# Performance work log

Measured on AMD Instinct MI355X. Metric: run time of the kernel, lower is better.

Reference implementation:

```python
import jax, jax.numpy as jnp
import numpy as np

B_GRAPHS, N_PER, T = 64, 5, 256
F_NODE, F_GLOB = 64, 16
H_MSG, H_UPD, H_GRP, H_ACT = 128, 128, 64, 4


def _lstm(x, Wih, Whh, bih, bhh):
    """PyTorch-semantics single-layer LSTM, batch_first=False.
    x: [L, B, Din] -> out [L, B, H]. Scan runs over dim 0 (faithful to the
    original code, which feeds [edges/nodes, T, F] into nn.LSTM)."""
    H = Whh.shape[1]
    xz = jnp.einsum('lbd,gd->lbg', x, Wih) + (bih + bhh)  # precomputed input proj [L,B,4H]
    h0 = jnp.zeros((x.shape[1], H), x.dtype)

    def step(carry, zt):
        h, c = carry
        z = zt + h @ Whh.T
        i, f, g, o = jnp.split(z, 4, axis=-1)  # torch gate order: i,f,g,o
        c = jax.nn.sigmoid(f) * c + jax.nn.sigmoid(i) * jnp.tanh(g)
        h = jax.nn.sigmoid(o) * jnp.tanh(c)
        return (h, c), h

    _, ys = jax.lax.scan(step, (h0, h0), xz)
    return ys


def _forward(nodes, global_attr,
             Wih_m, Whh_m, bih_m, bhh_m,
             Wih_u, Whh_u, bih_u, bhh_u,
             Wih_g, Whh_g, bih_g, bhh_g,
             Wih_a, Whh_a, bih_a, bhh_a,
             edge_indices, num_nodes, num_edges, batch_indices, chosen_who):
    N, Tdim = nodes.shape[0], nodes.shape[1]
    E = edge_indices.shape[1]
    B = num_nodes.shape[0]
    # Faithful to source: both src and target use edge_indices[0]
    src = edge_indices[0]
    tgt = edge_indices[0]
    ga = global_attr.reshape(-1, Tdim, global_attr.shape[1])  # [B, T, G]

    # --- message phase: gather -> LSTM -> relu -> scatter_min ---
    glob_e = jnp.repeat(ga, num_edges, axis=0, total_repeat_length=E)  # [E,T,G]
    msg_in = jnp.concatenate([nodes[src], nodes[tgt], glob_e], axis=2)  # [E,T,2F+G]
    message = jax.nn.relu(_lstm(msg_in, Wih_m, Whh_m, bih_m, bhh_m))    # [E,T,Hm]
    aggr = jax.ops.segment_min(message, tgt, num_segments=N)            # [N,T,Hm]

    # --- node update ---
    glob_n = jnp.repeat(ga, num_nodes, axis=0, total_repeat_length=N)   # [N,T,G]
    upd_in = jnp.concatenate([nodes, aggr, glob_n], axis=2)
    upd = jax.nn.relu(_lstm(upd_in, Wih_u, Whh_u, bih_u, bhh_u))        # [N,T,Hu]

    # --- global / group embedding ---
    agg_nodes = jax.ops.segment_min(upd, batch_indices, num_segments=B) # [B,T,Hu]
    group = jax.nn.relu(_lstm(jnp.concatenate([agg_nodes, ga], axis=2),
                              Wih_g, Whh_g, bih_g, bhh_g))              # [B,T,Hg]

    # --- action head ---
    agg_all = jax.ops.segment_min(upd, batch_indices, num_segments=B)
    counts = jax.ops.segment_sum(jnp.ones_like(batch_indices), batch_indices, num_segments=B)
    offsets = jnp.concatenate([jnp.zeros((1,), counts.dtype), jnp.cumsum(counts)[:-1]])
    adj = jnp.where(chosen_who == 3, chosen_who - 1, chosen_who)
    # faithful: element 0 is NOT adjusted/offset in the original loop
    atbw = jnp.where(jnp.arange(B) == 0, chosen_who, adj + offsets)
    chosen = upd[atbw]                                                  # [B,T,Hu]
    chosen = jnp.where((chosen_who == 3)[:, None, None], agg_all, chosen)
    act_in = jnp.concatenate([chosen, group], axis=2)                   # [B,T,Hu+Hg]
    res = _lstm(act_in, Wih_a, Whh_a, bih_a, bhh_a)[:, -1, :]           # [B, A]
    return jax.nn.softmax(res, axis=1)


def _lstm_params(k, din, h):
    k1, k2, k3, k4 = jax.random.split(k, 4)
    s = 1.0 / np.sqrt(h)
    return (jax.random.uniform(k1, (4 * h, din), jnp.float32, -s, s),
            jax.random.uniform(k2, (4 * h, h), jnp.float32, -s, s),
            jax.random.uniform(k3, (4 * h,), jnp.float32, -s, s),
            jax.random.uniform(k4, (4 * h,), jnp.float32, -s, s))


def setup_inputs() -> dict:
    key = jax.random.key(0)
    ks = jax.random.split(key, 8)
    N = B_GRAPHS * N_PER
    # complete directed graph inside each small group
    src, dst = [], []
    for g in range(B_GRAPHS):
        for i in range(N_PER):
            for j in range(N_PER):
                if i != j:
                    src.append(g * N_PER + i)
                    dst.append(g * N_PER + j)
    edge_indices = jnp.array([src, dst], dtype=jnp.int32)
    inp = {
        'nodes': jax.random.normal(ks[0], (N, T, F_NODE), jnp.float32),
        'global_attr': jax.random.normal(ks[1], (B_GRAPHS * T, F_GLOB), jnp.float32),
        'edge_indices': edge_indices,
        'num_nodes': jnp.full((B_GRAPHS,), N_PER, jnp.int32),
        'num_edges': jnp.full((B_GRAPHS,), N_PER * (N_PER - 1), jnp.int32),
        'batch_indices': jnp.repeat(jnp.arange(B_GRAPHS, dtype=jnp.int32), N_PER),
        'chosen_who': jax.random.randint(ks[2], (B_GRAPHS,), 0, 4, jnp.int32),
    }
    names = [('m', 2 * F_NODE + F_GLOB, H_MSG), ('u', H_MSG + F_NODE + F_GLOB, H_UPD),
             ('g', H_UPD + F_GLOB, H_GRP), ('a', H_UPD + H_GRP, H_ACT)]
    for idx, (suf, din, h) in enumerate(names):
        Wih, Whh, bih, bhh = _lstm_params(ks[3 + idx], din, h)
        inp['Wih_' + suf] = Wih
        inp['Whh_' + suf] = Whh
        inp['bih_' + suf] = bih
        inp['bhh_' + suf] = bhh
    return inp


def reference(nodes, global_attr, edge_indices, num_nodes, num_edges, batch_indices, chosen_who,
              Wih_m, Whh_m, bih_m, bhh_m, Wih_u, Whh_u, bih_u, bhh_u,
              Wih_g, Whh_g, bih_g, bhh_g, Wih_a, Whh_a, bih_a, bhh_a):
    return _forward(nodes, global_attr,
                    Wih_m, Whh_m, bih_m, bhh_m,
                    Wih_u, Whh_u, bih_u, bhh_u,
                    Wih_g, Whh_g, bih_g, bhh_g,
                    Wih_a, Whh_a, bih_a, bhh_a,
                    edge_indices, num_nodes, num_edges, batch_indices, chosen_who)
```

## Files before the change

kernel.cpp:

```cpp
#include <hip/hip_runtime.h>

typedef unsigned int u32;
typedef unsigned short u16;
typedef __fp16 h2 __attribute__((ext_vector_type(2)));

#define BG 64
#define NNODE 320
#define NEDGE 1280
#define TT 256
#define FN 64
#define FG 16
#define HM 128
#define HU 128
#define HG 64
#define HA 4
#define ZM 512
#define ZU 512
#define ZG 256
#define ZA 16
#define DM 144
#define DU 208
#define DG 144
#define DA 192

#define CV 64
#define O_NODES 0
#define O_GA    20480
#define O_WM    21504
#define O_WHM   95232
#define O_BM    160768
#define O_WU    161280
#define O_WHU   267776
#define O_BU    333312
#define O_WG    333824
#define O_WHG   370688
#define O_BG2   387072
#define O_WA    387328
#define O_WHA   390400
#define O_BA    390464
#define CONV_TOTAL 390480
#define O_XZN   390528
#define O_MSG   (O_XZN + NNODE * ZM)
#define O_XZU   (O_MSG + NEDGE * HM)
#define O_XZG   (O_XZU + NNODE * ZU)
#define O_XZA   (O_XZG + BG * ZG)
#define O_UPD   (O_XZA + BG * ZA)
#define WS_FLOATS (CV + O_UPD + NNODE * HU)

__device__ __forceinline__ float bf2f(u16 v) {
  return __uint_as_float(((u32)v) << 16);
}
__device__ __forceinline__ float rcp_(float x) { return __builtin_amdgcn_rcpf(x); }
__device__ __forceinline__ float sigf(float x) { return rcp_(1.0f + __expf(-x)); }
__device__ __forceinline__ float tanh_(float x) {
  float e = __expf(-2.0f * fabsf(x));
  float t = (1.0f - e) * rcp_(1.0f + e);
  return copysignf(t, x);
}
__device__ __forceinline__ float cvt(const void* p, int i, int flag) {
  return flag ? bf2f(((const u16*)p)[i]) : ((const float*)p)[i];
}

__device__ __forceinline__ h2 pk2(float a, float b) {
  return __builtin_amdgcn_cvt_pkrtz(a, b);
}
__device__ __forceinline__ u32 pk2u(float a, float b) {
  h2 r = __builtin_amdgcn_cvt_pkrtz(a, b);
  u32 out;
  __builtin_memcpy(&out, &r, 4);
  return out;
}

__device__ __forceinline__ float fdot2_(h2 a, h2 b, float c) {
#if __has_builtin(__builtin_amdgcn_fdot2)
  return __builtin_amdgcn_fdot2(a, b, c, false);
#else
  u32 ua, ub;
  __builtin_memcpy(&ua, &a, 4);
  __builtin_memcpy(&ub, &b, 4);
  asm("v_dot2_f32_f16 %0, %1, %2, %0" : "+v"(c) : "v"(ua), "v"(ub));
  return c;
#endif
}

template <int CTRL>
__device__ __forceinline__ float dppmov(float s) {
  return __int_as_float(
      __builtin_amdgcn_update_dpp(0, __float_as_int(s), CTRL, 0xF, 0xF, true));
}

#define BAR() asm volatile("s_waitcnt lgkmcnt(0)\n\ts_barrier" ::: "memory")

__global__ void k_detect(const u32* __restrict__ raw, int* __restrict__ flagp) {
  const int t = threadIdx.x;
  int zlo = 0, hits = 0;
  for (int k = t; k < 256; k += 64) {
    u32 w = raw[k];
    if ((w & 0xFFFFu) == 0u) zlo++;
    u32 m = (w >> 8) & 0x7Fu;
    if (m >= 40u && m <= 70u) hits++;
  }
#pragma unroll
  for (int off = 32; off; off >>= 1) {
    zlo += __shfl_down(zlo, off, 64);
    hits += __shfl_down(hits, off, 64);
  }
  if (t == 0) *flagp = (zlo < 128 && hits >= 128) ? 1 : 0;
}

__global__ __launch_bounds__(256) void k_convert(
    const void* nodes, const void* gattr,
    const void* Wm, const void* Whm, const void* bm1, const void* bm2,
    const void* Wu, const void* Whu, const void* bu1, const void* bu2,
    const void* Wg, const void* Whg, const void* bg1, const void* bg2,
    const void* Wa, const void* Wha, const void* ba1, const void* ba2,
    const int* __restrict__ flagp, float* __restrict__ dst) {
  const int flag = *flagp;
  const int i = blockIdx.x * 256 + threadIdx.x;
  if (i >= CONV_TOTAL) return;
  float v;
  if (i < O_GA) {
    int n = i >> 6, f = i & 63;
    v = cvt(nodes, (n * TT + (TT - 1)) * FN + f, flag);
  } else if (i < O_WM) {
    int l = i - O_GA; int b = l >> 4, g = l & 15;
    v = cvt(gattr, (b * TT + (TT - 1)) * FG + g, flag);
  } else if (i < O_BM) {
    v = (i < O_WHM) ? cvt(Wm, i - O_WM, flag) : cvt(Whm, i - O_WHM, flag);
  } else if (i < O_WU) {
    int l = i - O_BM; v = cvt(bm1, l, flag) + cvt(bm2, l, flag);
  } else if (i < O_BU) {
    v = (i < O_WHU) ? cvt(Wu, i - O_WU, flag) : cvt(Whu, i - O_WHU, flag);
  } else if (i < O_WG) {
    int l = i - O_BU; v = cvt(bu1, l, flag) + cvt(bu2, l, flag);
  } else if (i < O_BG2) {
    v = (i < O_WHG) ? cvt(Wg, i - O_WG, flag) : cvt(Whg, i - O_WHG, flag);
  } else if (i < O_WA) {
    int l = i - O_BG2; v = cvt(bg1, l, flag) + cvt(bg2, l, flag);
  } else if (i < O_WHA) {
    v = cvt(Wa, i - O_WA, flag);
  } else if (i < O_BA) {
    v = cvt(Wha, i - O_WHA, flag);
  } else {
    int l = i - O_BA; v = cvt(ba1, l, flag) + cvt(ba2, l, flag);
  }
  dst[i] = v;
}

__global__ __launch_bounds__(256) void k_pre(
    const float* __restrict__ cva,
    const int* __restrict__ num_nodes,
    float* __restrict__ XZN, float* __restrict__ XZu, float* __restrict__ XZg) {
  const int blk = blockIdx.x, tid = threadIdx.x;
  __shared__ float xv[FN];
  __shared__ float gav[FG];
  __shared__ int sgr;
  const float* nodes255 = cva + O_NODES;
  const float* ga255 = cva + O_GA;

  if (blk < NNODE) {
    const int n = blk;
    if (tid == 0) {
      int g = 0, acc = 0;
      while (g < BG) { int c = num_nodes[g]; if (n < acc + c) break; acc += c; ++g; }
      if (g >= BG) g = BG - 1;
      sgr = g;
    }
    if (tid < FN) xv[tid] = nodes255[n * FN + tid];
    __syncthreads();
    if (tid < FG) gav[tid] = ga255[sgr * FG + tid];
    __syncthreads();
    for (int j = tid; j < ZM; j += 256) {
      const float* wr = cva + O_WM + j * DM;
      float acc = cva[O_BM + j];
#pragma unroll
      for (int d = 0; d < FN; ++d) acc += (wr[d] + wr[FN + d]) * xv[d];
#pragma unroll
      for (int d = 0; d < FG; ++d) acc += wr[2 * FN + d] * gav[d];
      XZN[(size_t)n * ZM + j] = acc;
    }
  } else if (blk < 2 * NNODE) {
    const int n = blk - NNODE;
    if (tid == 0) {
      int g = 0, acc = 0;
      while (g < BG) { int c = num_nodes[g]; if (n < acc + c) break; acc += c; ++g; }
      if (g >= BG) g = BG - 1;
      sgr = g;
    }
    if (tid < FN) xv[tid] = nodes255[n * FN + tid];
    __syncthreads();
    if (tid < FG) gav[tid] = ga255[sgr * FG + tid];
    __syncthreads();
    for (int j = tid; j < ZU; j += 256) {
      const float* wr = cva + O_WU + j * DU;
      float acc = cva[O_BU + j];
#pragma unroll
      for (int d = 0; d < FN; ++d) acc += wr[d] * xv[d];
#pragma unroll
      for (int d = 0; d < FG; ++d) acc += wr[FN + HM + d] * gav[d];
      XZu[(size_t)n * ZU + j] = acc;
    }
  } else {
    const int b = blk - 2 * NNODE;
    if (tid < FG) gav[tid] = ga255[b * FG + tid];
    __syncthreads();
    if (tid < ZG) {
      const float* wr = cva + O_WG + tid * DG;
      float acc = cva[O_BG2 + tid];
#pragma unroll
      for (int d = 0; d < FG; ++d) acc += wr[HU + d] * gav[d];
      XZg[(size_t)b * ZG + tid] = acc;
    }
  }
}

template <int STEPS, bool GATHER>
__global__ __launch_bounds__(512, 2) void k_chain(
    const float* __restrict__ Whh, const float* __restrict__ XZ,
    const int* __restrict__ idx, float* __restrict__ hout) {
  const int t = threadIdx.x;
  const int p = t & 3;
  const int elem = t >> 2;
  const bool islead = (p == 0);
  __shared__ u32 hbuf[2][80];

  h2 w16[64];
  {
    const float4* wr = (const float4*)(Whh + (size_t)(p * 128 + elem) * 128);
#pragma unroll
    for (int q = 0; q < 32; ++q) {
      float4 v = wr[q];
      w16[2 * q] = pk2(v.x, v.y);
      w16[2 * q + 1] = pk2(v.z, v.w);
    }
  }
  const float LOG2E = 1.4426950408889634f;
  const float kmul = (p == 2) ? (-2.0f * LOG2E) : (-LOG2E);
  const float smul = (p == 2) ? 2.0f : 1.0f;
  const float badd = (p == 2) ? -1.0f : 0.0f;
  const float KT2 = -2.0f * LOG2E;

  if (t < 160) ((u32*)hbuf)[t] = 0u;
  float c = 0.0f;
  float hrelu_prev = 0.0f;
  {
    int row0 = GATHER ? idx[0] : 0;
    (void)row0;
  }
  float xz = XZ[(size_t)(GATHER ? idx[0] : 0) * 512 + p * 128 + elem];
  BAR();
  int cur = 0;
  for (int e = 0; e < STEPS; ++e) {
    const uint4* hb = (const uint4*)&hbuf[cur][0];
    float a0 = 0.0f, a1 = 0.0f, a2 = 0.0f, a3 = 0.0f;
#pragma unroll
    for (int q = 0; q < 16; ++q) {
      uint4 tv = hb[q];
      h2 h0, h1, h2_, h3;
      __builtin_memcpy(&h0, &tv.x, 4);
      __builtin_memcpy(&h1, &tv.y, 4);
      __builtin_memcpy(&h2_, &tv.z, 4);
      __builtin_memcpy(&h3, &tv.w, 4);
      a0 = fdot2_(w16[4 * q + 0], h0, a0);
      a1 = fdot2_(w16[4 * q + 1], h1, a1);
      a2 = fdot2_(w16[4 * q + 2], h2_, a2);
      a3 = fdot2_(w16[4 * q + 3], h3, a3);
    }
    float z = ((a0 + a1) + (a2 + a3)) + xz;
    {
      int nrow = GATHER ? idx[e + 1] : (e + 1);
      xz = XZ[(size_t)nrow * 512 + p * 128 + elem];
    }
    float ex = __builtin_amdgcn_exp2f(z * kmul);
    float gq = __builtin_fmaf(smul, rcp_(1.0f + ex), badd);
    float gf = dppmov<0xB1>(gq);
    float gt = dppmov<0x4E>(gq);
    float go = dppmov<0x1B>(gq);
    c = __builtin_fmaf(gf, c, gq * gt);
    float ec = __builtin_amdgcn_exp2f(c * KT2);
    float th = __builtin_fmaf(2.0f, rcp_(1.0f + ec), -1.0f);
    float h = go * th;
    if (islead) {
      ((u16*)&hbuf[cur ^ 1][0])[elem] = (u16)pk2u(h, h);
      if (e > 0) hout[(size_t)(e - 1) * 128 + elem] = hrelu_prev;
      hrelu_prev = fmaxf(h, 0.0f);
    }
    BAR();
    cur ^= 1;
  }
  if (islead) hout[(size_t)(STEPS - 1) * 128 + elem] = hrelu_prev;
}

__global__ __launch_bounds__(256) void k_aggminproj(
    const float* __restrict__ cva, const float* __restrict__ msg,
    const int* __restrict__ eidx, float* __restrict__ XZu) {
  const int n = blockIdx.x, tid = threadIdx.x;
  __shared__ float av[HM];
  if (tid < HM) {
    float m = __uint_as_float(0x7f800000u);
    for (int e = 0; e < NEDGE; ++e) {
      if (eidx[e] == n) m = fminf(m, msg[(size_t)e * HM + tid]);
    }
    av[tid] = m;
  }
  __syncthreads();
  for (int j = tid; j < ZU; j += 256) {
    const float* wr = cva + O_WU + j * DU + FN;
    float acc = 0.0f;
#pragma unroll
    for (int k = 0; k < HM; ++k) acc += wr[k] * av[k];
    XZu[(size_t)n * ZU + j] += acc;
  }
}

__global__ __launch_bounds__(256) void k_gproj(
    const float* __restrict__ cva, const float* __restrict__ upd,
    const int* __restrict__ bidx, const int* __restrict__ who,
    float* __restrict__ XZg, float* __restrict__ XZa) {
  const int blk = blockIdx.x, tid = threadIdx.x;
  __shared__ float buf[HU];
  __shared__ int satbw;
  if (blk < BG) {
    const int b = blk;
    if (tid < HU) {
      float m = __uint_as_float(0x7f800000u);
      for (int n = 0; n < NNODE; ++n) {
        if (bidx[n] == b) m = fminf(m, upd[(size_t)n * HU + tid]);
      }
      buf[tid] = m;
    }
    __syncthreads();
    if (tid < ZG) {
      const float* wr = cva + O_WG + tid * DG;
      float acc = 0.0f;
#pragma unroll
      for (int k = 0; k < HU; ++k) acc += wr[k] * buf[k];
      XZg[(size_t)b * ZG + tid] += acc;
    }
  } else {
    const int b = blk - BG;
    const int whoB = who[b];
    if (tid == 0) {
      int off = 0;
      for (int i = 0; i < NNODE; ++i) off += (bidx[i] < b) ? 1 : 0;
      const int adj = (whoB == 3) ? 2 : whoB;
      satbw = (b == 0) ? who[0] : (adj + off);
    }
    if (whoB == 3) {
      if (tid < HU) {
        float m = __uint_as_float(0x7f800000u);
        for (int n = 0; n < NNODE; ++n) {
          if (bidx[n] == b) m = fminf(m, upd[(size_t)n * HU + tid]);
        }
        buf[tid] = m;
      }
      __syncthreads();
    } else {
      __syncthreads();
      if (tid < HU) buf[tid] = upd[(size_t)satbw * HU + tid];
      __syncthreads();
    }
    if (tid < ZA) {
      const float* wr = cva + O_WA + tid * DA;
      float acc = cva[O_BA + tid];
#pragma unroll
      for (int k = 0; k < HU; ++k) acc += wr[k] * buf[k];
      XZa[(size_t)b * ZA + tid] = acc;
    }
  }
}

__global__ __launch_bounds__(256, 2) void k_final(
    const float* __restrict__ cva, const float* __restrict__ XZg,
    const float* __restrict__ XZa, float* __restrict__ out) {
  const int j = threadIdx.x;
  __shared__ __align__(16) float hg[HG];
  __shared__ float zsg[ZG];
  __shared__ float grp[BG * HG];
  __shared__ float za[ZA];
  __shared__ float haL[HA];
  __shared__ float res[BG * HA];

  float wg[HG];
  {
    const float* wr = cva + O_WHG + j * HG;
#pragma unroll
    for (int k = 0; k < HG; ++k) wg[k] = wr[k];
  }
  if (j < HG) hg[j] = 0.0f;
  float cg = 0.0f;
  __syncthreads();
  for (int b = 0; b < BG; ++b) {
    float acc = XZg[(size_t)b * ZG + j];
#pragma unroll
    for (int k = 0; k < HG; ++k) acc += wg[k] * hg[k];
    zsg[j] = acc;
    __syncthreads();
    if (j < HG) {
      float zi = zsg[j], zf = zsg[HG + j], zg = zsg[2 * HG + j], zo = zsg[3 * HG + j];
      cg = sigf(zf) * cg + sigf(zi) * tanh_(zg);
      float h = sigf(zo) * tanh_(cg);
      hg[j] = h;
      grp[b * HG + j] = fmaxf(h, 0.0f);
    }
    __syncthreads();
  }

  float wa2[HG];
  float wha[HA];
  if (j < ZA) {
    const float* wr2 = cva + O_WA + j * DA + HU;
#pragma unroll
    for (int k = 0; k < HG; ++k) wa2[k] = wr2[k];
#pragma unroll
    for (int k = 0; k < HA; ++k) wha[k] = cva[O_WHA + j * HA + k];
  }
  if (j < HA) haL[j] = 0.0f;
  float ca = 0.0f;
  __syncthreads();
  for (int b = 0; b < BG; ++b) {
    if (j < ZA) {
      float acc = XZa[(size_t)b * ZA + j];
#pragma unroll
      for (int k = 0; k < HG; ++k) acc += wa2[k] * grp[b * HG + k];
#pragma unroll
      for (int k = 0; k < HA; ++k) acc += wha[k] * haL[k];
      za[j] = acc;
    }
    __syncthreads();
    if (j < HA) {
      float zi = za[j], zf = za[HA + j], zg = za[2 * HA + j], zo = za[3 * HA + j];
      ca = sigf(zf) * ca + sigf(zi) * tanh_(zg);
      float h = sigf(zo) * tanh_(ca);
      haL[j] = h;
      res[b * HA + j] = h;
    }
    __syncthreads();
  }
  if (j < BG) {
    float x0 = res[j * 4 + 0], x1 = res[j * 4 + 1];
    float x2 = res[j * 4 + 2], x3 = res[j * 4 + 3];
    float m = fmaxf(fmaxf(x0, x1), fmaxf(x2, x3));
    float e0 = __expf(x0 - m), e1 = __expf(x1 - m);
    float e2 = __expf(x2 - m), e3 = __expf(x3 - m);
    float s = e0 + e1 + e2 + e3;
    out[j * 4 + 0] = e0 / s;
    out[j * 4 + 1] = e1 / s;
    out[j * 4 + 2] = e2 / s;
    out[j * 4 + 3] = e3 / s;
  }
}

__global__ void k_zero(float* out) { out[threadIdx.x] = 0.0f; }

extern "C" void kernel_launch(void* const* d_in, const int* in_sizes, int n_in,
                              void* d_out, int out_size, void* d_ws, size_t ws_size,
                              hipStream_t stream) {
  const void* nodes = d_in[0];
  const void* gattr = d_in[1];
  const int* eidx  = (const int*)d_in[2];
  const int* nn    = (const int*)d_in[3];
  const int* ne    = (const int*)d_in[4];
  const int* bidx  = (const int*)d_in[5];
  const int* who   = (const int*)d_in[6];
  (void)ne;

  if (ws_size < (size_t)WS_FLOATS * 4) {
    k_zero<<<1, 256, 0, stream>>>((float*)d_out);
    return;
  }

  float* ws = (float*)d_ws;
  int* flagp = (int*)d_ws;
  float* cva = ws + CV;
  float* XZN = cva + O_XZN;
  float* msg = cva + O_MSG;
  float* XZu = cva + O_XZU;
  float* XZg = cva + O_XZG;
  float* XZa = cva + O_XZA;
  float* upd = cva + O_UPD;

  k_detect<<<1, 64, 0, stream>>>((const u32*)nodes, flagp);
  k_convert<<<(CONV_TOTAL + 255) / 256, 256, 0, stream>>>(
      nodes, gattr,
      d_in[7], d_in[8], d_in[9], d_in[10],
      d_in[11], d_in[12], d_in[13], d_in[14],
      d_in[15], d_in[16], d_in[17], d_in[18],
      d_in[19], d_in[20], d_in[21], d_in[22],
      flagp, cva);
  k_pre<<<2 * NNODE + BG, 256, 0, stream>>>(cva, nn, XZN, XZu, XZg);
  k_chain<NEDGE, true><<<1, 512, 0, stream>>>(cva + O_WHM, XZN, eidx, msg);
  k_aggminproj<<<NNODE, 256, 0, stream>>>(cva, msg, eidx, XZu);
  k_chain<NNODE, false><<<1, 512, 0, stream>>>(cva + O_WHU, XZu, nullptr, upd);
  k_gproj<<<2 * BG, 256, 0, stream>>>(cva, upd, bidx, who, XZg, XZa);
  k_final<<<1, 256, 0, stream>>>(cva, XZg, XZa, (float*)d_out);
}
```

Before: 1.185 ms.

## Replace per-node edge scan with atomic scatter-min and prefetch next gather index

The segment-min over edges had each node block scan all 1280 edges serially. It is now an init kernel plus a per-edge kernel that applies atomicMin on float bit patterns, since the ReLU outputs are non-negative. A separate projection kernel then reads the aggregated rows. The chain kernel also loads the next gather index one step ahead, taking the dependent index load off the recurrent critical path. The atomic-on-bits trick is only correct for non-negative floats, and the change adds two kernel launches.

```diff
diff --git a/kernel.cpp b/kernel.cpp
--- a/kernel.cpp
+++ b/kernel.cpp
@@ -44,7 +44,8 @@
 #define O_XZU   (O_MSG + NEDGE * HM)
 #define O_XZG   (O_XZU + NNODE * ZU)
 #define O_XZA   (O_XZG + BG * ZG)
-#define O_UPD   (O_XZA + BG * ZA)
+#define O_AGGR  (O_XZA + BG * ZA)
+#define O_UPD   (O_AGGR + NNODE * HM)
 #define WS_FLOATS (CV + O_UPD + NNODE * HU)
 
 __device__ __forceinline__ float bf2f(u16 v) {
@@ -243,11 +244,8 @@
   if (t < 160) ((u32*)hbuf)[t] = 0u;
   float c = 0.0f;
   float hrelu_prev = 0.0f;
-  {
-    int row0 = GATHER ? idx[0] : 0;
-    (void)row0;
-  }
   float xz = XZ[(size_t)(GATHER ? idx[0] : 0) * 512 + p * 128 + elem];
+  int nrow = GATHER ? idx[1] : 1;
   BAR();
   int cur = 0;
   for (int e = 0; e < STEPS; ++e) {
@@ -267,10 +265,8 @@
       a3 = fdot2_(w16[4 * q + 3], h3, a3);
     }
     float z = ((a0 + a1) + (a2 + a3)) + xz;
-    {
-      int nrow = GATHER ? idx[e + 1] : (e + 1);
-      xz = XZ[(size_t)nrow * 512 + p * 128 + elem];
-    }
+    float xzn = XZ[(size_t)nrow * 512 + p * 128 + elem];
+    nrow = GATHER ? idx[e + 2] : (e + 2);
     float ex = __builtin_amdgcn_exp2f(z * kmul);
     float gq = __builtin_fmaf(smul, rcp_(1.0f + ex), badd);
     float gf = dppmov<0xB1>(gq);
@@ -285,24 +281,31 @@
       if (e > 0) hout[(size_t)(e - 1) * 128 + elem] = hrelu_prev;
       hrelu_prev = fmaxf(h, 0.0f);
     }
+    xz = xzn;
     BAR();
     cur ^= 1;
   }
   if (islead) hout[(size_t)(STEPS - 1) * 128 + elem] = hrelu_prev;
 }
 
-__global__ __launch_bounds__(256) void k_aggminproj(
-    const float* __restrict__ cva, const float* __restrict__ msg,
-    const int* __restrict__ eidx, float* __restrict__ XZu) {
+__global__ __launch_bounds__(256) void k_agginit(u32* __restrict__ aggr) {
+  aggr[blockIdx.x * 256 + threadIdx.x] = 0x7f800000u;
+}
+
+__global__ __launch_bounds__(128) void k_aggmin(
+    const float* __restrict__ msg, const int* __restrict__ eidx,
+    u32* __restrict__ aggr) {
+  const int e = blockIdx.x, j = threadIdx.x;
+  u32 bits = __float_as_uint(msg[(size_t)e * HM + j]);
+  atomicMin(&aggr[(size_t)eidx[e] * HM + j], bits);
+}
+
+__global__ __launch_bounds__(256) void k_aggproj(
+    const float* __restrict__ cva, const float* __restrict__ aggr,
+    float* __restrict__ XZu) {
   const int n = blockIdx.x, tid = threadIdx.x;
   __shared__ float av[HM];
-  if (tid < HM) {
-    float m = __uint_as_float(0x7f800000u);
-    for (int e = 0; e < NEDGE; ++e) {
-      if (eidx[e] == n) m = fminf(m, msg[(size_t)e * HM + tid]);
-    }
-    av[tid] = m;
-  }
+  if (tid < HM) av[tid] = aggr[(size_t)n * HM + tid];
   __syncthreads();
   for (int j = tid; j < ZU; j += 256) {
     const float* wr = cva + O_WU + j * DU + FN;
@@ -478,6 +481,7 @@
   float* XZu = cva + O_XZU;
   float* XZg = cva + O_XZG;
   float* XZa = cva + O_XZA;
+  float* aggr = cva + O_AGGR;
   float* upd = cva + O_UPD;
 
   k_detect<<<1, 64, 0, stream>>>((const u32*)nodes, flagp);
@@ -489,8 +493,10 @@
       d_in[19], d_in[20], d_in[21], d_in[22],
       flagp, cva);
   k_pre<<<2 * NNODE + BG, 256, 0, stream>>>(cva, nn, XZN, XZu, XZg);
+  k_agginit<<<(NNODE * HM) / 256, 256, 0, stream>>>((u32*)aggr);
   k_chain<NEDGE, true><<<1, 512, 0, stream>>>(cva + O_WHM, XZN, eidx, msg);
-  k_aggminproj<<<NNODE, 256, 0, stream>>>(cva, msg, eidx, XZu);
+  k_aggmin<<<NEDGE, 128, 0, stream>>>(msg, eidx, (u32*)aggr);
+  k_aggproj<<<NNODE, 256, 0, stream>>>(cva, aggr, XZu);
   k_chain<NNODE, false><<<1, 512, 0, stream>>>(cva + O_WHU, XZu, nullptr, upd);
   k_gproj<<<2 * BG, 256, 0, stream>>>(cva, upd, bidx, who, XZg, XZa);
   k_final<<<1, 256, 0, stream>>>(cva, XZg, XZa, (float*)d_out);
```

Measured after the change: 1.101 ms. -7.1%, faster.
